# Optimization experiments

Measured on AMD Instinct MI355X. Metric: run time of the kernel, lower is better.

Reference implementation:

```python
import jax, jax.numpy as jnp
import numpy as np

THRESHOLD = 0.005
EPS = 1e-5  # torch instance_norm default eps


def setup_inputs() -> dict:
    key = jax.random.key(0)
    k1, k2, k3 = jax.random.split(key, 3)
    B, C, H, W = 4, 64, 64, 64
    feat = 64
    stdv = 1.0 / np.sqrt(feat)  # matches __init_W_bias__ uniform(-stdv, stdv)
    x = jax.random.normal(k1, (B, C, H, W), dtype=jnp.float32)
    W0 = jax.random.uniform(k2, (1, feat, feat), dtype=jnp.float32, minval=-stdv, maxval=stdv)
    W1 = jax.random.uniform(k3, (1, feat, feat), dtype=jnp.float32, minval=-stdv, maxval=stdv)
    return {"x": x, "W0": W0, "W1": W1}


def _laplacian(xn):
    # xn: [B, N, C] node features (pixels x channels). Built under no_grad in torch.
    norms = jnp.sqrt(jnp.sum(xn * xn, axis=2, keepdims=True))  # [B, N, 1]
    num = jnp.einsum('bnc,bmc->bnm', xn, xn)                    # [B, N, N]
    corr = num / (norms * jnp.swapaxes(norms, 1, 2))
    # relu then threshold -> binary adjacency (threshold > 0, so relu is subsumed)
    A = (corr > THRESHOLD).astype(xn.dtype)
    deg = jnp.sum(A, axis=2)                                    # [B, N]
    d_is = 1.0 / jnp.sqrt(deg)                                  # inverse(sqrt(D)) is diagonal
    return A * d_is[:, :, None] * d_is[:, None, :]              # D^-1/2 A D^-1/2


def _instance_norm(h):
    # torch F.instance_norm on [B, N, F] normalizes over the last dim per (b, n)
    mean = jnp.mean(h, axis=-1, keepdims=True)
    var = jnp.mean((h - mean) ** 2, axis=-1, keepdims=True)
    return (h - mean) / jnp.sqrt(var + EPS)


def reference(x, W0, W1):
    B, C, H, Wd = x.shape
    x_linear = x.reshape(B, C, H * Wd).transpose(0, 2, 1)  # [B, N, C]
    lap = _laplacian(jax.lax.stop_gradient(x_linear))       # adjacency built with no_grad
    for Wk in (W0, W1):
        lx = jnp.einsum('bnm,bmc->bnc', lap, x_linear)      # laplacian diffusion
        h = jnp.einsum('bnc,cf->bnf', lx, Wk[0])            # shared weight (repeat over batch)
        x_linear = jax.nn.relu(_instance_norm(h))
    return x_linear
```

## Files before the change

### kernel.cpp

```cpp
#include <hip/hip_runtime.h>
#include <hip/hip_bf16.h>
#include <cstdint>

#define BB 4
#define CC 64
#define NN 4096
#define NWRD 64
#define TAU 0.005f
#define EPSN 1e-5f

typedef __attribute__((ext_vector_type(8))) short short8;
typedef __attribute__((ext_vector_type(4))) float f32x4;
typedef unsigned long long ull;

__device__ inline unsigned int bf16_rne(float v) {
    unsigned int u = __float_as_uint(v);
    return (u + 0x7FFFu + ((u >> 16) & 1u)) >> 16;
}

__device__ inline void gload_lds16(const void* g, void* lds_base) {
    __builtin_amdgcn_global_load_lds(
        (const __attribute__((address_space(1))) unsigned int*)g,
        (__attribute__((address_space(3))) unsigned int*)lds_base, 16, 0, 0);
}


__global__ __launch_bounds__(256) void k_transpose(const float* __restrict__ x,
                                                   unsigned short* __restrict__ ynh,
                                                   unsigned short* __restrict__ ynl,
                                                   int* __restrict__ deg) {
    __shared__ float lds[64 * 65];
    int t = threadIdx.x;
    int b = blockIdx.y;
    int n0 = blockIdx.x * 64;
    int gid = (b * (NN / 64) + blockIdx.x) * 256 + t;
    if (gid < BB * NN) deg[gid] = 0;
    #pragma unroll
    for (int i = 0; i < 4; ++i) {
        int c = i * 16 + (t >> 4);
        int nc = (t & 15) * 4;
        float4 v = *(const float4*)(x + ((size_t)(b * CC + c)) * NN + n0 + nc);
        lds[c * 65 + nc + 0] = v.x;
        lds[c * 65 + nc + 1] = v.y;
        lds[c * 65 + nc + 2] = v.z;
        lds[c * 65 + nc + 3] = v.w;
    }
    __syncthreads();
    int l = t & 63, wv = t >> 6;
    for (int i = 0; i < 16; ++i) {
        int n = wv * 16 + i;
        float v = lds[l * 65 + n];
        float s = v * v;
        #pragma unroll
        for (int off = 32; off; off >>= 1) s += __shfl_xor(s, off, 64);
        float yv = v * rsqrtf(s);
        unsigned int hb = bf16_rne(yv);
        float lo = yv - __uint_as_float(hb << 16);
        unsigned int lb = bf16_rne(lo);
        size_t row = (size_t)(b * NN + n0 + n);
        ynh[row * CC + l] = (unsigned short)hb;
        ynl[row * CC + l] = (unsigned short)lb;
    }
}

#define CORR_MC 128
__global__ __launch_bounds__(256) void k_corr(const unsigned short* __restrict__ ynh,
                                              const unsigned short* __restrict__ ynl,
                                              ull* __restrict__ mask,
                                              int* __restrict__ deg) {
    __shared__ unsigned short ldsH[2][CORR_MC * 64];
    __shared__ unsigned short ldsL[2][CORR_MC * 64];
    int t = threadIdx.x;
    int l = t & 63, wv = t >> 6;
    int lc = l & 15, q = l >> 4;
    int b = blockIdx.z;
    int idx = blockIdx.x, I = 0;
    while (idx >= 16 - I) { idx -= 16 - I; ++I; }
    int J = I + idx;
    int n0 = I * 256 + wv * 64;
    int m0 = J * 256;
    const unsigned short* bH = ynh + (size_t)b * NN * CC;
    const unsigned short* bL = ynl + (size_t)b * NN * CC;

    short8 ah[4][2], al[4][2];
    #pragma unroll
    for (int nt = 0; nt < 4; ++nt)
        #pragma unroll
        for (int ks = 0; ks < 2; ++ks) {
            size_t off = (size_t)(n0 + nt * 16 + lc) * CC + (ks * 4 + q) * 8;
            ah[nt][ks] = *(const short8*)(bH + off);
            al[nt][ks] = *(const short8*)(bL + off);
        }

    int rr = l & 15;
    int rsel = rr & 3;
    int qq = rr >> 2;
    int myq = l >> 4;

    auto stage = [&](int mc, int bufi) {
        int mbase = m0 + mc * CORR_MC;
        #pragma unroll
        for (int rd = 0; rd < 4; ++rd) {
            int gu = rd * 256 + wv * 64;
            int g = gu + l;
            int ci = (g & ~7) | ((g & 7) ^ ((g >> 3) & 7));
            gload_lds16(bH + (size_t)mbase * CC + ci * 8, &ldsH[bufi][gu * 8]);
            gload_lds16(bL + (size_t)mbase * CC + ci * 8, &ldsL[bufi][gu * 8]);
        }
    };

    ull wout[4];
    int degacc = 0;
    stage(0, 0);
    for (int mc = 0; mc < 2; ++mc) {
        __syncthreads();
        if (mc == 0) stage(1, 1);
        int bufi = mc & 1;
        ull w0 = 0, w1 = 0;
        #pragma unroll
        for (int tt = 0; tt < 8; ++tt) {
            short8 bh[2], bl[2];
            #pragma unroll
            for (int ks = 0; ks < 2; ++ks) {
                int rowm = tt * 16 + lc;
                int sw = ((ks * 4 + q) ^ (rowm & 7)) * 8;
                bh[ks] = *(const short8*)&ldsH[bufi][rowm * 64 + sw];
                bl[ks] = *(const short8*)&ldsL[bufi][rowm * 64 + sw];
            }
            #pragma unroll
            for (int nt = 0; nt < 4; ++nt) {
                f32x4 acc = {0.f, 0.f, 0.f, 0.f};
                #pragma unroll
                for (int ks = 0; ks < 2; ++ks) {
                    acc = __builtin_amdgcn_mfma_f32_16x16x32_bf16(ah[nt][ks], bh[ks], acc, 0, 0, 0);
                    acc = __builtin_amdgcn_mfma_f32_16x16x32_bf16(ah[nt][ks], bl[ks], acc, 0, 0, 0);
                    acc = __builtin_amdgcn_mfma_f32_16x16x32_bf16(al[nt][ks], bh[ks], acc, 0, 0, 0);
                }
                ull bal[4];
                #pragma unroll
                for (int r = 0; r < 4; ++r)
                    bal[r] = __ballot(acc[r] > TAU);
                ull sa = (rsel & 1) ? bal[1] : bal[0];
                ull sb = (rsel & 1) ? bal[3] : bal[2];
                ull sel = (rsel & 2) ? sb : sa;
                ull part = ((sel >> (qq * 16)) & 0xFFFFull) << ((tt & 3) * 16);
                if (myq == nt) { if (tt < 4) w0 |= part; else w1 |= part; }
            }
        }
        wout[mc * 2 + 0] = w0;
        wout[mc * 2 + 1] = w1;
        degacc += __popcll(w0) + __popcll(w1);
    }

    int row = b * NN + n0 + l;
    #pragma unroll
    for (int c = 0; c < 4; ++c)
        mask[((size_t)(b * NWRD + J * 4 + c)) * NN + n0 + l] = wout[c];
    atomicAdd(&deg[row], degacc);

    if (J > I) {
        __syncthreads();
        ull* sh = (ull*)&ldsH[0][0];
        #pragma unroll
        for (int c = 0; c < 4; ++c) sh[(wv * 64 + l) * 5 + c] = wout[c];
        __syncthreads();
        const ull Mv[6] = {0x00000000FFFFFFFFull, 0x0000FFFF0000FFFFull,
                           0x00FF00FF00FF00FFull, 0x0F0F0F0F0F0F0F0Full,
                           0x3333333333333333ull, 0x5555555555555555ull};
        int dm = 0;
        ull tw[4];
        #pragma unroll
        for (int a = 0; a < 4; ++a) {
            ull xv = sh[(a * 64 + l) * 5 + wv];
            int dd = 32;
            #pragma unroll
            for (int s = 0; s < 6; ++s, dd >>= 1) {
                ull y = __shfl_xor(xv, dd, 64);
                ull M = Mv[s];
                xv = (l & dd) ? ((xv & ~M) | ((y >> dd) & M))
                              : ((xv & M) | ((y << dd) & ~M));
            }
            tw[a] = xv;
            dm += __popcll(xv);
        }
        int mrow = b * NN + J * 256 + wv * 64 + l;
        #pragma unroll
        for (int a = 0; a < 4; ++a)
            mask[((size_t)(b * NWRD + I * 4 + a)) * NN + J * 256 + wv * 64 + l] = tw[a];
        atomicAdd(&deg[mrow], dm);
    }
}

__global__ __launch_bounds__(256) void k_pack(const float* __restrict__ x,
                                              const int* __restrict__ deg,
                                              unsigned short* __restrict__ yph) {
    __shared__ float lp[32 * 65];
    int t = threadIdx.x;
    int kt = blockIdx.x;
    int b = blockIdx.y;
    #pragma unroll
    for (int i = 0; i < 2; ++i) {
        int idx = i * 256 + t;
        int c = idx >> 3;
        int nq = (idx & 7) * 4;
        float4 v = *(const float4*)(x + ((size_t)(b * CC + c)) * NN + kt * 32 + nq);
        lp[(nq + 0) * 65 + c] = v.x;
        lp[(nq + 1) * 65 + c] = v.y;
        lp[(nq + 2) * 65 + c] = v.z;
        lp[(nq + 3) * 65 + c] = v.w;
    }
    __syncthreads();
    size_t obase = (size_t)b * NN * CC + (size_t)kt * 2048;
    int kin = t & 31;
    int chi = t >> 5;
    float d = rsqrtf((float)deg[b * NN + kt * 32 + kin]);
    #pragma unroll
    for (int g8 = 0; g8 < 8; ++g8) {
        int c = g8 * 8 + chi;
        yph[obase + c * 32 + kin] = (unsigned short)bf16_rne(lp[kin * 65 + c] * d);
    }
}

__global__ __launch_bounds__(512, 4) void k_fused(const ull* __restrict__ mask,
                                                  const unsigned short* __restrict__ yph,
                                                  const int* __restrict__ deg,
                                                  const float* __restrict__ W,
                                                  float* __restrict__ xout,
                                                  unsigned short* __restrict__ xpack) {
    __shared__ __align__(16) float red[8 * 32][68];

    int t = threadIdx.x;
    int l = t & 63, wv = t >> 6;
    int lc = l & 15, q = l >> 4;
    int b = blockIdx.y;
    int n0 = blockIdx.x * 32;
    const unsigned short* src = yph + (size_t)b * NN * CC;

    f32x4 acc[2][4];
    #pragma unroll
    for (int nt = 0; nt < 2; ++nt)
        #pragma unroll
        for (int tt = 0; tt < 4; ++tt) acc[nt][tt] = f32x4{0.f, 0.f, 0.f, 0.f};

    #pragma unroll
    for (int ch = 0; ch < 8; ++ch) {
        ull mwc[2];
        #pragma unroll
        for (int nt = 0; nt < 2; ++nt)
            mwc[nt] = mask[((size_t)(b * NWRD + wv * 8 + ch)) * NN + n0 + nt * 16 + lc];
        int g0 = wv * 16 + ch * 2;
        #pragma unroll
        for (int kt = 0; kt < 2; ++kt) {
            const unsigned short* bsrc = src + (size_t)(g0 + kt) * 2048;
            short8 bf[4];
            #pragma unroll
            for (int tt = 0; tt < 4; ++tt)
                bf[tt] = *(const short8*)&bsrc[(tt * 16 + lc) * 32 + q * 8];
            union { unsigned int u[4]; short8 v; } a[2];
            #pragma unroll
            for (int nt = 0; nt < 2; ++nt) {
                unsigned int bits = (unsigned int)(mwc[nt] >> (kt * 32 + q * 8)) & 0xFFu;
                #pragma unroll
                for (int j = 0; j < 4; ++j)
                    a[nt].u[j] = ((bits >> (2 * j)) & 1u ? 0x3F80u : 0u)
                               | ((bits >> (2 * j + 1)) & 1u ? 0x3F800000u : 0u);
            }
            #pragma unroll
            for (int tt = 0; tt < 4; ++tt)
                #pragma unroll
                for (int nt = 0; nt < 2; ++nt)
                    acc[nt][tt] = __builtin_amdgcn_mfma_f32_16x16x32_bf16(a[nt].v, bf[tt], acc[nt][tt], 0, 0, 0);
        }
    }

    #pragma unroll
    for (int nt = 0; nt < 2; ++nt)
        #pragma unroll
        for (int tt = 0; tt < 4; ++tt)
            #pragma unroll
            for (int r = 0; r < 4; ++r)
                red[wv * 32 + nt * 16 + q * 4 + r][tt * 16 + lc] = acc[nt][tt][r];
    __syncthreads();

    {
        int n = t >> 4, c0 = (t & 15) * 4;
        float dRow = rsqrtf((float)deg[b * NN + n0 + n]);
        float s[4] = {0.f, 0.f, 0.f, 0.f};
        #pragma unroll
        for (int w = 0; w < 8; ++w) {
            const float* rp = &red[w * 32 + n][c0];
            #pragma unroll
            for (int j = 0; j < 4; ++j) s[j] += rp[j];
        }
        float* wp = &red[n][c0];
        #pragma unroll
        for (int j = 0; j < 4; ++j) wp[j] = s[j] * dRow;
    }
    __syncthreads();

    float Wreg[64];
    #pragma unroll
    for (int c = 0; c < 64; ++c) Wreg[c] = W[c * 64 + l];
    ull xv = 0;
    #pragma unroll
    for (int tI = 0; tI < 4; ++tI) {
        int nn = wv * 4 + tI;
        int grow = b * NN + n0 + nn;
        float h = 0.f;
        #pragma unroll
        for (int c4 = 0; c4 < 16; ++c4) {
            float4 s4 = *(const float4*)&red[nn][c4 * 4];
            h += s4.x * Wreg[c4 * 4 + 0] + s4.y * Wreg[c4 * 4 + 1]
               + s4.z * Wreg[c4 * 4 + 2] + s4.w * Wreg[c4 * 4 + 3];
        }
        float mean = h;
        #pragma unroll
        for (int off = 32; off; off >>= 1) mean += __shfl_xor(mean, off, 64);
        mean *= (1.f / 64.f);
        float dv = h - mean;
        float var = dv * dv;
        #pragma unroll
        for (int off = 32; off; off >>= 1) var += __shfl_xor(var, off, 64);
        var *= (1.f / 64.f);
        float o = dv * rsqrtf(var + EPSN);
        o = o > 0.f ? o : 0.f;
        if (xout)
            xout[(size_t)grow * CC + l] = o;
        if (xpack) {
            float dR = rsqrtf((float)deg[grow]);
            xv |= (ull)(unsigned short)bf16_rne(o * dR) << (16 * tI);
        }
    }
    if (xpack) {
        size_t base = (size_t)b * NN * CC + (size_t)(n0 >> 5) * 2048
                    + (size_t)l * 32 + (size_t)wv * 4;
        *(ull*)&xpack[base] = xv;
    }
}

extern "C" void kernel_launch(void* const* d_in, const int* in_sizes, int n_in,
                              void* d_out, int out_size, void* d_ws, size_t ws_size,
                              hipStream_t stream) {
    const float* x  = (const float*)d_in[0];
    const float* W0 = (const float*)d_in[1];
    const float* W1 = (const float*)d_in[2];
    float* out = (float*)d_out;

    char* ws = (char*)d_ws;
    ull* mask = (ull*)(ws);
    unsigned short* ynh = (unsigned short*)(ws + ((size_t)8 << 20));
    unsigned short* ynl = (unsigned short*)(ws + ((size_t)10 << 20));
    unsigned short* xp0 = (unsigned short*)(ws + ((size_t)12 << 20));
    unsigned short* xp1 = (unsigned short*)(ws + ((size_t)14 << 20));
    int* deg = (int*)(ws + ((size_t)16 << 20));

    k_transpose<<<dim3(NN / 64, BB), 256, 0, stream>>>(x, ynh, ynl, deg);
    k_corr<<<dim3(136, 1, BB), 256, 0, stream>>>(ynh, ynl, mask, deg);

    k_pack<<<dim3(128, BB), 256, 0, stream>>>(x, deg, xp0);
    k_fused<<<dim3(NN / 32, BB), 512, 0, stream>>>(mask, xp0, deg, W0, nullptr, xp1);

    k_fused<<<dim3(NN / 32, BB), 512, 0, stream>>>(mask, xp1, deg, W1, out, nullptr);
}
```

Measured before the change: 142.2 us.

## Merge pack and both graph layers into one cooperative kernel with grid syncs

Replaces the three kernels k_pack, k_fused (W0) and k_fused (W1) with one cooperative kernel of 256 persistent blocks. Each block handles two tiles per phase, and grid-wide syncs separate the phases. This removes two launch boundaries and their drain and fill gaps. In exchange it halves the number of blocks in flight per phase, adds grid-sync cost, and adds an extra __syncthreads before the shared reduction buffer is reused.

```diff
diff --git a/kernel.cpp b/kernel.cpp
--- a/kernel.cpp
+++ b/kernel.cpp
@@ -1,6 +1,9 @@
 #include <hip/hip_runtime.h>
 #include <hip/hip_bf16.h>
+#include <hip/hip_cooperative_groups.h>
 #include <cstdint>
+
+namespace cg = cooperative_groups;
 
 #define BB 4
 #define CC 64
@@ -191,49 +194,17 @@
     }
 }
 
-__global__ __launch_bounds__(256) void k_pack(const float* __restrict__ x,
-                                              const int* __restrict__ deg,
-                                              unsigned short* __restrict__ yph) {
-    __shared__ float lp[32 * 65];
-    int t = threadIdx.x;
-    int kt = blockIdx.x;
-    int b = blockIdx.y;
-    #pragma unroll
-    for (int i = 0; i < 2; ++i) {
-        int idx = i * 256 + t;
-        int c = idx >> 3;
-        int nq = (idx & 7) * 4;
-        float4 v = *(const float4*)(x + ((size_t)(b * CC + c)) * NN + kt * 32 + nq);
-        lp[(nq + 0) * 65 + c] = v.x;
-        lp[(nq + 1) * 65 + c] = v.y;
-        lp[(nq + 2) * 65 + c] = v.z;
-        lp[(nq + 3) * 65 + c] = v.w;
-    }
-    __syncthreads();
-    size_t obase = (size_t)b * NN * CC + (size_t)kt * 2048;
-    int kin = t & 31;
-    int chi = t >> 5;
-    float d = rsqrtf((float)deg[b * NN + kt * 32 + kin]);
-    #pragma unroll
-    for (int g8 = 0; g8 < 8; ++g8) {
-        int c = g8 * 8 + chi;
-        yph[obase + c * 32 + kin] = (unsigned short)bf16_rne(lp[kin * 65 + c] * d);
-    }
-}
-
-__global__ __launch_bounds__(512, 4) void k_fused(const ull* __restrict__ mask,
-                                                  const unsigned short* __restrict__ yph,
-                                                  const int* __restrict__ deg,
-                                                  const float* __restrict__ W,
-                                                  float* __restrict__ xout,
-                                                  unsigned short* __restrict__ xpack) {
-    __shared__ __align__(16) float red[8 * 32][68];
-
-    int t = threadIdx.x;
+
+__device__ __forceinline__ void fused_layer(const ull* __restrict__ mask,
+                                            const unsigned short* __restrict__ yph,
+                                            const int* __restrict__ deg,
+                                            const float* __restrict__ W,
+                                            float* __restrict__ xout,
+                                            unsigned short* __restrict__ xpack,
+                                            int b, int n0, int t,
+                                            float (*red)[68]) {
     int l = t & 63, wv = t >> 6;
     int lc = l & 15, q = l >> 4;
-    int b = blockIdx.y;
-    int n0 = blockIdx.x * 32;
     const unsigned short* src = yph + (size_t)b * NN * CC;
 
     f32x4 acc[2][4];
@@ -273,6 +244,7 @@
         }
     }
 
+    __syncthreads();
     #pragma unroll
     for (int nt = 0; nt < 2; ++nt)
         #pragma unroll
@@ -338,6 +310,59 @@
     }
 }
 
+__global__ __launch_bounds__(512, 4) void k_back(const float* __restrict__ x,
+                                                 const float* __restrict__ W0,
+                                                 const float* __restrict__ W1,
+                                                 float* __restrict__ out,
+                                                 const ull* __restrict__ mask,
+                                                 unsigned short* __restrict__ xp0,
+                                                 unsigned short* __restrict__ xp1,
+                                                 const int* __restrict__ deg) {
+    __shared__ __align__(16) float red[8 * 32][68];
+    cg::grid_group grid = cg::this_grid();
+    int t = threadIdx.x;
+    int bid = blockIdx.x;
+
+    #pragma unroll
+    for (int i = 0; i < 2; ++i) {
+        int u = bid + i * 256;
+        int b = u >> 7, kt = u & 127;
+        float* lp = (float*)red;
+        if (i) __syncthreads();
+        int c = t >> 3;
+        int nq = (t & 7) * 4;
+        float4 v = *(const float4*)(x + ((size_t)(b * CC + c)) * NN + kt * 32 + nq);
+        lp[(nq + 0) * 65 + c] = v.x;
+        lp[(nq + 1) * 65 + c] = v.y;
+        lp[(nq + 2) * 65 + c] = v.z;
+        lp[(nq + 3) * 65 + c] = v.w;
+        __syncthreads();
+        size_t obase = (size_t)b * NN * CC + (size_t)kt * 2048;
+        int kin = t & 31;
+        int chi = t >> 5;
+        float d = rsqrtf((float)deg[b * NN + kt * 32 + kin]);
+        #pragma unroll
+        for (int g4 = 0; g4 < 4; ++g4) {
+            int cc = g4 * 16 + chi;
+            xp0[obase + cc * 32 + kin] = (unsigned short)bf16_rne(lp[kin * 65 + cc] * d);
+        }
+    }
+    grid.sync();
+
+    #pragma unroll
+    for (int i = 0; i < 2; ++i) {
+        int u = bid + i * 256;
+        fused_layer(mask, xp0, deg, W0, nullptr, xp1, u >> 7, (u & 127) * 32, t, red);
+    }
+    grid.sync();
+
+    #pragma unroll
+    for (int i = 0; i < 2; ++i) {
+        int u = bid + i * 256;
+        fused_layer(mask, xp1, deg, W1, out, nullptr, u >> 7, (u & 127) * 32, t, red);
+    }
+}
+
 extern "C" void kernel_launch(void* const* d_in, const int* in_sizes, int n_in,
                               void* d_out, int out_size, void* d_ws, size_t ws_size,
                               hipStream_t stream) {
@@ -357,8 +382,8 @@
     k_transpose<<<dim3(NN / 64, BB), 256, 0, stream>>>(x, ynh, ynl, deg);
     k_corr<<<dim3(136, 1, BB), 256, 0, stream>>>(ynh, ynl, mask, deg);
 
-    k_pack<<<dim3(128, BB), 256, 0, stream>>>(x, deg, xp0);
-    k_fused<<<dim3(NN / 32, BB), 512, 0, stream>>>(mask, xp0, deg, W0, nullptr, xp1);
-
-    k_fused<<<dim3(NN / 32, BB), 512, 0, stream>>>(mask, xp1, deg, W1, out, nullptr);
-}
+    void* args[] = {(void*)&x, (void*)&W0, (void*)&W1, (void*)&out,
+                    (void*)&mask, (void*)&xp0, (void*)&xp1, (void*)&deg};
+    hipLaunchCooperativeKernel((const void*)k_back, dim3(256), dim3(512),
+                               args, 0, stream);
+}
```

New measurement: 280.6 us. 1.97x slower.
